# Kernel tuning notes

Hardware: AMD Instinct MI355X
Metric: run time of the kernel (lower is better)

The kernel has to match this reference:

```python
import jax, jax.numpy as jnp
import numpy as np

E, H, I = 16, 2048, 768
B, S = 4, 1024
TOPK = 8
BLK_R, BLK_C = 128, 128


def blockwise_dequantize(w, scale_inv, r, c):
    # w: [E, M, N] (fp8 values stored as fp32 here), scale_inv: [E, M//r, N//c]
    e, m, n = w.shape
    wb = w.reshape(e, m // r, r, n // c, c)
    wb = wb * scale_inv[:, :, None, :, None]
    return wb.reshape(e, m, n)


def setup_inputs() -> dict:
    key = jax.random.key(0)
    ks = jax.random.split(key, 7)
    return {
        "hidden_states": jax.random.normal(ks[0], (B, S, H), dtype=jnp.float32),
        "routing_weights": jax.random.uniform(ks[1], (B * S, E), dtype=jnp.float32),
        "gate_up_proj": jax.random.normal(ks[2], (E, H, 2 * I), dtype=jnp.float32),
        "gate_up_proj_scale_inv": jax.random.uniform(ks[3], (E, H // BLK_R, 2 * I // BLK_C), dtype=jnp.float32),
        "down_proj": jax.random.normal(ks[4], (E, I, H), dtype=jnp.float32),
        "down_proj_scale_inv": jax.random.uniform(ks[5], (E, I // BLK_R, H // BLK_C), dtype=jnp.float32),
        "router_indices": jax.random.randint(ks[6], (B * S, TOPK), 0, E, dtype=jnp.int64 if jax.config.jax_enable_x64 else jnp.int32),
    }


def reference(hidden_states, routing_weights, gate_up_proj, gate_up_proj_scale_inv,
              down_proj, down_proj_scale_inv, router_indices):
    batch_size = hidden_states.shape[0]
    hs = hidden_states.reshape(-1, H)                      # [T, H], T = B*S
    x = jnp.broadcast_to(hs[None], (E,) + hs.shape)        # repeat across experts

    gu_w = blockwise_dequantize(gate_up_proj, gate_up_proj_scale_inv, BLK_R, BLK_C)   # [E, H, 2I]
    dn_w = blockwise_dequantize(down_proj, down_proj_scale_inv, BLK_R, BLK_C)         # [E, I, H]

    gate_up = jnp.einsum('eth,ehf->etf', x, gu_w)          # [E, T, 2I]
    gate, up = jnp.split(gate_up, 2, axis=-1)
    inter = up * jax.nn.silu(gate)                         # [E, T, I]
    next_states = jnp.einsum('eti,eih->eth', inter, dn_w)  # [E, T, H]

    next_states = next_states.reshape(E, batch_size, -1, H)
    rw = routing_weights.T.reshape(E, batch_size, -1)      # [E, B, S]
    out = (next_states * rw[..., None]).sum(axis=0)        # [B, S, H]
    return out
```

## Files before the change

kernel.cpp:

```cpp
#include <hip/hip_runtime.h>
#include <hip/hip_bf16.h>
#include <cstdint>

#define E_     16
#define H_     2048
#define I_     768
#define T_     4096
#define TWO_I  1536
#define K2_    (E_ * I_)

typedef __bf16 bf16x8 __attribute__((ext_vector_type(8)));
typedef float  floatx4 __attribute__((ext_vector_type(4)));

__device__ __forceinline__ void gload_lds16(const void* g, void* l) {
  __builtin_amdgcn_global_load_lds(
      (const __attribute__((address_space(1))) void*)(void*)g,
      (__attribute__((address_space(3))) void*)l,
      16, 0, 0);
}

#define ASM_VMCNT(n) asm volatile("s_waitcnt vmcnt(" #n ")" ::: "memory")
#define ASM_LGKM0()  asm volatile("s_waitcnt lgkmcnt(0)" ::: "memory")
#define SBAR()       __builtin_amdgcn_s_barrier()
#define SCHED0()     __builtin_amdgcn_sched_barrier(0)

__global__ void k_convert(const float* __restrict__ in, __bf16* __restrict__ out) {
  size_t idx = ((size_t)blockIdx.x * blockDim.x + threadIdx.x) * 8;
  float4 a = *(const float4*)(in + idx);
  float4 b = *(const float4*)(in + idx + 4);
  bf16x8 o;
  o[0] = (__bf16)a.x; o[1] = (__bf16)a.y; o[2] = (__bf16)a.z; o[3] = (__bf16)a.w;
  o[4] = (__bf16)b.x; o[5] = (__bf16)b.y; o[6] = (__bf16)b.z; o[7] = (__bf16)b.w;
  *(bf16x8*)(out + idx) = o;
}

__global__ void k_dq_transpose(const float* __restrict__ src, __bf16* __restrict__ dst,
                               const float* __restrict__ scale, int R, int C,
                               size_t slab, size_t rowStride, int ilvHalf) {
  const int e  = blockIdx.z;
  const int n0 = blockIdx.x * 64;
  const int m0 = blockIdx.y * 64;
  __shared__ float tile[64 * 65];
  const float s = scale[((size_t)e * (R >> 7) + (m0 >> 7)) * (C >> 7) + (n0 >> 7)];
  const float* sp = src + ((size_t)e * R + m0) * C + n0;
  const int t  = threadIdx.x;
  const int c4 = (t & 15) * 4;
  const int rb = t >> 4;
  #pragma unroll
  for (int p = 0; p < 4; ++p) {
    int r = p * 16 + rb;
    float4 v = *(const float4*)(sp + (size_t)r * C + c4);
    tile[(c4 + 0) * 65 + r] = v.x * s;
    tile[(c4 + 1) * 65 + r] = v.y * s;
    tile[(c4 + 2) * 65 + r] = v.z * s;
    tile[(c4 + 3) * 65 + r] = v.w * s;
  }
  __syncthreads();
  const int c8 = (t & 7) * 8;
  const int r0 = t >> 3;
  #pragma unroll
  for (int p = 0; p < 2; ++p) {
    int nr = r0 + p * 32;
    int ng = n0 + nr;
    int np;
    if (ilvHalf) {
      int h = (ng >= ilvHalf) ? 1 : 0;
      int iLoc = ng - h * ilvHalf;
      np = ((iLoc >> 5) << 6) + h * 32 + (iLoc & 31);
    } else {
      np = ng;
    }
    const float* row = &tile[nr * 65 + c8];
    bf16x8 o;
    #pragma unroll
    for (int j = 0; j < 8; ++j) o[j] = (__bf16)row[j];
    *(bf16x8*)(dst + (size_t)e * slab + (size_t)np * rowStride + m0 + c8) = o;
  }
}


#define STG_A(tt, h) do { int b_ = ((tt)&1)*16384 + (h)*8192; \
    gload_lds16(aSrc + (size_t)((h)*128)*LDK + (tt)*64, dA + b_); \
    gload_lds16(aSrc + (size_t)((h)*128 + 64)*LDK + (tt)*64, dA + b_ + 4096); } while (0)
#define STG_B(tt, h) do { int b_ = ((tt)&1)*16384 + (h)*8192; \
    gload_lds16(bSrc + (size_t)((h)*128)*LDK + (tt)*64, dB + b_); \
    gload_lds16(bSrc + (size_t)((h)*128 + 64)*LDK + (tt)*64, dB + b_ + 4096); } while (0)

#define AF4(MI0) do { \
    af[0][0] = *(const bf16x8*)(pA + (MI0)*1024 + kc0); \
    af[0][1] = *(const bf16x8*)(pA + (MI0)*1024 + kc1); \
    af[1][0] = *(const bf16x8*)(pA + ((MI0)+1)*1024 + kc0); \
    af[1][1] = *(const bf16x8*)(pA + ((MI0)+1)*1024 + kc1); } while (0)

#define MFMA16(MI0) do { \
    _Pragma("unroll") \
    for (int ii = 0; ii < 2; ++ii) { \
      _Pragma("unroll") \
      for (int ni = 0; ni < 4; ++ni) { \
        acc[(MI0)+ii][ni] = __builtin_amdgcn_mfma_f32_16x16x32_bf16(af[ii][0], bb[ni][0], acc[(MI0)+ii][ni], 0, 0, 0); \
        acc[(MI0)+ii][ni] = __builtin_amdgcn_mfma_f32_16x16x32_bf16(af[ii][1], bb[ni][1], acc[(MI0)+ii][ni], 0, 0, 0); \
      } \
    } } while (0)

#define PHASE(MI0, STAGE_STMT, CKPT_STMT) do { \
    AF4(MI0); \
    STAGE_STMT; \
    CKPT_STMT; \
    SBAR(); \
    ASM_LGKM0(); \
    SCHED0(); \
    __builtin_amdgcn_s_setprio(1); \
    MFMA16(MI0); \
    __builtin_amdgcn_s_setprio(0); \
    SBAR(); \
  } while (0)

__global__ __launch_bounds__(512, 2)
void k_gemm1(const __bf16* __restrict__ A, const __bf16* __restrict__ W,
             const float* __restrict__ rw, __bf16* __restrict__ inter) {
  extern __shared__ __align__(16) __bf16 smem[];
  __bf16* sA = smem;
  __bf16* sB = smem + 32768;
  float*  sRW = (float*)(smem + 65536);

  const int e  = blockIdx.z;
  const int m0 = blockIdx.x * 256;
  const int by = blockIdx.y;
  const int n0 = by * 256;
  const int t    = threadIdx.x;
  const int wave = t >> 6, lane = t & 63;
  const int wm = wave >> 2, wn = wave & 3;
  const int l4 = lane >> 4, r16 = lane & 15;
  const int LDK = H_;

  if (t < 256) sRW[t] = rw[(size_t)(m0 + t) * E_ + e];
  ASM_VMCNT(0);

  const int rowSt = t >> 3;
  const int kcSt  = ((t & 7) ^ ((t >> 3) & 7)) << 3;
  const __bf16* aSrc = A + (size_t)(m0 + rowSt) * H_ + kcSt;
  const __bf16* bSrc = W + ((size_t)e * TWO_I + n0 + rowSt) * H_ + kcSt;
  __bf16* dA = sA + wave * 512;
  __bf16* dB = sB + wave * 512;

  const int kc0 = (l4 ^ (r16 & 7)) << 3;
  const int kc1 = ((4 + l4) ^ (r16 & 7)) << 3;
  const __bf16* pArd = sA + wm * 8192 + r16 * 64;
  const __bf16* pBrd = sB + (wn >> 1) * 8192 + ((wn & 1) * 64 + r16) * 64;

  floatx4 acc[8][4];
  #pragma unroll
  for (int mi = 0; mi < 8; ++mi)
    #pragma unroll
    for (int ni = 0; ni < 4; ++ni) {
      floatx4 z = {0.f, 0.f, 0.f, 0.f};
      acc[mi][ni] = z;
    }

  STG_B(0, 0); STG_B(0, 1); STG_A(0, 0); STG_A(0, 1);
  STG_B(1, 0); STG_B(1, 1);
  ASM_VMCNT(4);
  SBAR();

  const int NT = H_ / 64;
  for (int tt = 0; tt < NT; ++tt) {
    const int bo = (tt & 1) * 16384;
    const __bf16* pA = pArd + bo;
    const __bf16* pB = pBrd + bo;
    bf16x8 bb[4][2], af[2][2];
    #pragma unroll
    for (int ni = 0; ni < 4; ++ni) {
      bb[ni][0] = *(const bf16x8*)(pB + ni * 1024 + kc0);
      bb[ni][1] = *(const bf16x8*)(pB + ni * 1024 + kc1);
    }
    PHASE(0, if (tt + 1 < NT) STG_A(tt + 1, 0), (void)0);
    PHASE(2, if (tt + 1 < NT) STG_A(tt + 1, 1), (void)0);
    PHASE(4, if (tt + 2 < NT) STG_B(tt + 2, 0), (void)0);
    PHASE(6, if (tt + 2 < NT) STG_B(tt + 2, 1),
             if (tt + 2 < NT) { ASM_VMCNT(4); } else { ASM_VMCNT(0); });
  }

  const int rq = l4 * 4;
  const int gBase = (by * 4 + wn) * 32;
  #pragma unroll
  for (int mi = 0; mi < 8; ++mi) {
    const int rl = wm * 128 + mi * 16 + rq;
    #pragma unroll
    for (int ni = 0; ni < 2; ++ni) {
      const size_t colIdx = (size_t)e * I_ + gBase + ni * 16 + r16;
      #pragma unroll
      for (int r = 0; r < 4; ++r) {
        float g = acc[mi][ni][r];
        float u = acc[mi][ni + 2][r];
        float sil = g / (1.0f + __expf(-g));
        float val = u * sil * sRW[rl + r];
        inter[(size_t)(m0 + rl + r) * K2_ + colIdx] = (__bf16)val;
      }
    }
  }
}

__global__ __launch_bounds__(512, 2)
void k_gemm2(const __bf16* __restrict__ Ainter, const __bf16* __restrict__ W,
             float* __restrict__ out) {
  extern __shared__ __align__(16) __bf16 smem[];
  __bf16* sA = smem;
  __bf16* sB = smem + 32768;

  const int m0 = blockIdx.x * 256;
  const int n0 = blockIdx.y * 256;
  const size_t kOff = (size_t)blockIdx.z * (K2_ / 2);
  const int t    = threadIdx.x;
  const int wave = t >> 6, lane = t & 63;
  const int wm = wave >> 2, wn = wave & 3;
  const int l4 = lane >> 4, r16 = lane & 15;
  const int LDK = K2_;

  const int rowSt = t >> 3;
  const int kcSt  = ((t & 7) ^ ((t >> 3) & 7)) << 3;
  const __bf16* aSrc = Ainter + (size_t)(m0 + rowSt) * K2_ + kOff + kcSt;
  const __bf16* bSrc = W      + (size_t)(n0 + rowSt) * K2_ + kOff + kcSt;
  __bf16* dA = sA + wave * 512;
  __bf16* dB = sB + wave * 512;

  const int kc0 = (l4 ^ (r16 & 7)) << 3;
  const int kc1 = ((4 + l4) ^ (r16 & 7)) << 3;
  const __bf16* pArd = sA + wm * 8192 + r16 * 64;
  const __bf16* pBrd = sB + (wn >> 1) * 8192 + ((wn & 1) * 64 + r16) * 64;

  floatx4 acc[8][4];
  #pragma unroll
  for (int mi = 0; mi < 8; ++mi)
    #pragma unroll
    for (int ni = 0; ni < 4; ++ni) {
      floatx4 z = {0.f, 0.f, 0.f, 0.f};
      acc[mi][ni] = z;
    }

  STG_B(0, 0); STG_B(0, 1); STG_A(0, 0); STG_A(0, 1);
  STG_B(1, 0); STG_B(1, 1);
  ASM_VMCNT(4);
  SBAR();

  const int NT = (K2_ / 2) / 64;
  for (int tt = 0; tt < NT; ++tt) {
    const int bo = (tt & 1) * 16384;
    const __bf16* pA = pArd + bo;
    const __bf16* pB = pBrd + bo;
    bf16x8 bb[4][2], af[2][2];
    #pragma unroll
    for (int ni = 0; ni < 4; ++ni) {
      bb[ni][0] = *(const bf16x8*)(pB + ni * 1024 + kc0);
      bb[ni][1] = *(const bf16x8*)(pB + ni * 1024 + kc1);
    }
    PHASE(0, if (tt + 1 < NT) STG_A(tt + 1, 0), (void)0);
    PHASE(2, if (tt + 1 < NT) STG_A(tt + 1, 1), (void)0);
    PHASE(4, if (tt + 2 < NT) STG_B(tt + 2, 0), (void)0);
    PHASE(6, if (tt + 2 < NT) STG_B(tt + 2, 1),
             if (tt + 2 < NT) { ASM_VMCNT(4); } else { ASM_VMCNT(0); });
  }

  const int rq = l4 * 4;
  #pragma unroll
  for (int mi = 0; mi < 8; ++mi) {
    const int rl = wm * 128 + mi * 16 + rq;
    #pragma unroll
    for (int ni = 0; ni < 4; ++ni) {
      const int cl = wn * 64 + ni * 16 + r16;
      #pragma unroll
      for (int r = 0; r < 4; ++r)
        unsafeAtomicAdd(out + (size_t)(m0 + rl + r) * H_ + n0 + cl, acc[mi][ni][r]);
    }
  }
}

extern "C" void kernel_launch(void* const* d_in, const int* in_sizes, int n_in,
                              void* d_out, int out_size, void* d_ws, size_t ws_size,
                              hipStream_t stream) {
  const float* hs   = (const float*)d_in[0];
  const float* rw   = (const float*)d_in[1];
  const float* gup  = (const float*)d_in[2];
  const float* gups = (const float*)d_in[3];
  const float* dnp  = (const float*)d_in[4];
  const float* dnps = (const float*)d_in[5];
  float* out = (float*)d_out;

  char* ws = (char*)d_ws;
  __bf16* hsb  = (__bf16*)ws;
  __bf16* wgu  = (__bf16*)(ws + (size_t)(16 << 20));
  __bf16* wdn  = (__bf16*)(ws + (size_t)(112 << 20));
  __bf16* intr = (__bf16*)(ws + (size_t)(160 << 20));

  static int inited = 0;
  if (!inited) {
    hipFuncSetAttribute((const void*)k_gemm1,
                        hipFuncAttributeMaxDynamicSharedMemorySize, 132096);
    hipFuncSetAttribute((const void*)k_gemm2,
                        hipFuncAttributeMaxDynamicSharedMemorySize, 131072);
    inited = 1;
  }

  hipMemsetAsync(out, 0, (size_t)T_ * H_ * sizeof(float), stream);

  k_convert<<<(T_ * H_) / (256 * 8), 256, 0, stream>>>(hs, hsb);
  k_dq_transpose<<<dim3(TWO_I / 64, H_ / 64, E_), 256, 0, stream>>>(
      gup, wgu, gups, H_, TWO_I, (size_t)TWO_I * H_, (size_t)H_, I_);
  k_dq_transpose<<<dim3(H_ / 64, I_ / 64, E_), 256, 0, stream>>>(
      dnp, wdn, dnps, I_, H_, (size_t)I_, (size_t)K2_, 0);
  k_gemm1<<<dim3(T_ / 256, TWO_I / 256, E_), 512, 132096, stream>>>(hsb, wgu, rw, intr);
  k_gemm2<<<dim3(T_ / 256, H_ / 256, 2), 512, 131072, stream>>>(intr, wdn, out);
}
```

Measured before the change: 927.6 us.

## Remap block IDs for XCD locality and replace atomic split-K with partial buffer

Both GEMM kernels remap the linear block index so that consecutive blocks scheduled round-robin across the 8 XCDs work on the same expert or output region, aiming to improve L2 reuse of A and W tiles. GEMM2 stops zeroing the output and using atomic adds. Each split-K half now writes plainly to its own buffer (output or a workspace partial that reuses the gate-up weight region, which is dead by then), and a new elementwise kernel sums them. This drops the memset and atomic traffic but adds a 32MB partial write/read pass and an extra launch.

Result: no change. 920.3 us (-0.8%).

```diff
diff --git a/kernel.cpp b/kernel.cpp
--- a/kernel.cpp
+++ b/kernel.cpp
@@ -78,7 +78,6 @@
   }
 }
 
-
 #define STG_A(tt, h) do { int b_ = ((tt)&1)*16384 + (h)*8192; \
     gload_lds16(aSrc + (size_t)((h)*128)*LDK + (tt)*64, dA + b_); \
     gload_lds16(aSrc + (size_t)((h)*128 + 64)*LDK + (tt)*64, dA + b_ + 4096); } while (0)
@@ -123,10 +122,14 @@
   __bf16* sB = smem + 32768;
   float*  sRW = (float*)(smem + 65536);
 
-  const int e  = blockIdx.z;
-  const int m0 = blockIdx.x * 256;
-  const int by = blockIdx.y;
+  const int lid = blockIdx.x + 16 * (blockIdx.y + 6 * blockIdx.z);
+  const int nid = (lid & 7) * 192 + (lid >> 3);
+  const int e  = nid / 96;
+  const int r_ = nid - e * 96;
+  const int by = r_ >> 4;
+  const int m0 = (r_ & 15) * 256;
   const int n0 = by * 256;
+
   const int t    = threadIdx.x;
   const int wave = t >> 6, lane = t & 63;
   const int wm = wave >> 2, wn = wave & 3;
@@ -202,14 +205,20 @@
 
 __global__ __launch_bounds__(512, 2)
 void k_gemm2(const __bf16* __restrict__ Ainter, const __bf16* __restrict__ W,
-             float* __restrict__ out) {
+             float* __restrict__ out0, float* __restrict__ out1) {
   extern __shared__ __align__(16) __bf16 smem[];
   __bf16* sA = smem;
   __bf16* sB = smem + 32768;
 
-  const int m0 = blockIdx.x * 256;
-  const int n0 = blockIdx.y * 256;
-  const size_t kOff = (size_t)blockIdx.z * (K2_ / 2);
+  const int lid = blockIdx.x + 16 * (blockIdx.y + 8 * blockIdx.z);
+  const int nid = (lid & 7) * 32 + (lid >> 3);
+  const int bz = nid >> 7;
+  const int r_ = nid & 127;
+  const int n0 = (r_ >> 4) * 256;
+  const int m0 = (r_ & 15) * 256;
+  float* dst = bz ? out1 : out0;
+  const size_t kOff = (size_t)bz * (K2_ / 2);
+
   const int t    = threadIdx.x;
   const int wave = t >> 6, lane = t & 63;
   const int wm = wave >> 2, wn = wave & 3;
@@ -269,9 +278,17 @@
       const int cl = wn * 64 + ni * 16 + r16;
       #pragma unroll
       for (int r = 0; r < 4; ++r)
-        unsafeAtomicAdd(out + (size_t)(m0 + rl + r) * H_ + n0 + cl, acc[mi][ni][r]);
-    }
-  }
+        dst[(size_t)(m0 + rl + r) * H_ + n0 + cl] = acc[mi][ni][r];
+    }
+  }
+}
+
+__global__ void k_addout(float* __restrict__ out, const float* __restrict__ part) {
+  size_t i = ((size_t)blockIdx.x * blockDim.x + threadIdx.x) * 4;
+  float4 a = *(const float4*)(out + i);
+  float4 b = *(const float4*)(part + i);
+  a.x += b.x; a.y += b.y; a.z += b.z; a.w += b.w;
+  *(float4*)(out + i) = a;
 }
 
 extern "C" void kernel_launch(void* const* d_in, const int* in_sizes, int n_in,
@@ -290,6 +307,7 @@
   __bf16* wgu  = (__bf16*)(ws + (size_t)(16 << 20));
   __bf16* wdn  = (__bf16*)(ws + (size_t)(112 << 20));
   __bf16* intr = (__bf16*)(ws + (size_t)(160 << 20));
+  float* part = (float*)(ws + (size_t)(16 << 20));
 
   static int inited = 0;
   if (!inited) {
@@ -300,13 +318,12 @@
     inited = 1;
   }
 
-  hipMemsetAsync(out, 0, (size_t)T_ * H_ * sizeof(float), stream);
-
   k_convert<<<(T_ * H_) / (256 * 8), 256, 0, stream>>>(hs, hsb);
   k_dq_transpose<<<dim3(TWO_I / 64, H_ / 64, E_), 256, 0, stream>>>(
       gup, wgu, gups, H_, TWO_I, (size_t)TWO_I * H_, (size_t)H_, I_);
   k_dq_transpose<<<dim3(H_ / 64, I_ / 64, E_), 256, 0, stream>>>(
       dnp, wdn, dnps, I_, H_, (size_t)I_, (size_t)K2_, 0);
   k_gemm1<<<dim3(T_ / 256, TWO_I / 256, E_), 512, 132096, stream>>>(hsb, wgu, rw, intr);
-  k_gemm2<<<dim3(T_ / 256, H_ / 256, 2), 512, 131072, stream>>>(intr, wdn, out);
-}
+  k_gemm2<<<dim3(T_ / 256, H_ / 256, 2), 512, 131072, stream>>>(intr, wdn, out, part);
+  k_addout<<<(T_ * H_) / (256 * 4), 256, 0, stream>>>(out, part);
+}
```
